# Performance work log

Hardware: AMD Instinct MI355X
Metric: run time of the kernel (lower is better)

## Reference

```python
import jax, jax.numpy as jnp
import numpy as np

N_TREES, N_LEAVES, PATH_LEN, N_NODES, D, B = 10, 16, 5, 31, 256, 4096


def _local_paths():
    # root-to-leaf paths of a full binary tree, depth 4: 31 nodes, 16 leaves, path len 5
    return np.array([[0, 1 + l // 8, 3 + l // 4, 7 + l // 2, 15 + l]
                     for l in range(N_LEAVES)], np.int32)


def setup_inputs() -> dict:
    key = jax.random.key(0)
    k1, k2, k3, k4, k5, k6 = jax.random.split(key, 6)
    # one activated leaf per tree -> multi-hot cross_features (B, N_TREES*N_LEAVES)
    leaf = jax.random.randint(k1, (B, N_TREES), 0, N_LEAVES)
    cross = jnp.zeros((B, N_TREES, N_LEAVES), jnp.float32)
    cross = cross.at[jnp.arange(B)[:, None], jnp.arange(N_TREES)[None, :], leaf].set(1.0)
    cross_features = cross.reshape(B, N_TREES * N_LEAVES)
    # learned params: node embedding table + single-layer LSTM (torch init scale 1/sqrt(D))
    emb = jax.random.normal(k2, (N_TREES * N_NODES, D), jnp.float32) * 0.02
    s = 1.0 / np.sqrt(D)
    W_ih = jax.random.uniform(k3, (4 * D, D), jnp.float32, -s, s)
    W_hh = jax.random.uniform(k4, (4 * D, D), jnp.float32, -s, s)
    b_ih = jax.random.uniform(k5, (4 * D,), jnp.float32, -s, s)
    b_hh = jax.random.uniform(k6, (4 * D,), jnp.float32, -s, s)
    return {"cross_features": cross_features, "emb": emb, "W_ih": W_ih,
            "W_hh": W_hh, "b_ih": b_ih, "b_hh": b_hh}


def reference(cross_features, emb, W_ih, W_hh, b_ih, b_hh):
    # global path node ids per (tree, leaf): [T, L, P]
    gpaths = jnp.asarray(_local_paths())[None, :, :] + \
        (jnp.arange(N_TREES, dtype=jnp.int32) * N_NODES)[:, None, None]
    # activated leaf per tree (exactly one hot per 16-leaf block)
    leaf = jnp.argmax(cross_features.reshape(B, N_TREES, N_LEAVES), axis=-1)  # [B, T]
    node_ids = gpaths[jnp.arange(N_TREES)[None, :], leaf]                     # [B, T, P]
    x = emb[node_ids].reshape(B * N_TREES, PATH_LEN, D)                       # packed paths
    # precompute input projections for all steps: [N, P, 4D]
    xg = jnp.einsum('npd,gd->npg', x, W_ih) + (b_ih + b_hh)

    def step(carry, xt):
        h, c = carry
        g = xt + h @ W_hh.T
        i, f, gg, o = jnp.split(g, 4, axis=-1)  # torch gate order: i, f, g, o
        c = jax.nn.sigmoid(f) * c + jax.nn.sigmoid(i) * jnp.tanh(gg)
        h = jax.nn.sigmoid(o) * jnp.tanh(c)
        return (h, c), None

    n = B * N_TREES
    h0 = jnp.zeros((n, D), x.dtype)
    (h, _), _ = jax.lax.scan(step, (h0, h0), jnp.swapaxes(xg, 0, 1))
    return h.reshape(B, N_TREES, D)
```

## Files before the change

### kernel.cpp

```cpp
#include <hip/hip_runtime.h>

#define NT 10
#define NL 16
#define NN 31
#define DD 256
#define G4 1024
#define NNODES (NT*NN)
#define NPATH (NT*NL)
#define NB 4096

__device__ unsigned g_tf[3][NT][32];

__device__ __forceinline__ float sigf(float x)   { return 1.0f / (1.0f + __expf(-x)); }
__device__ __forceinline__ float tanh_f(float x) { return 2.0f / (1.0f + __expf(-2.0f*x)) - 1.0f; }

__device__ __forceinline__ void co_store(float* p, float v) {
    union { float f; unsigned u; } c; c.f = v;
    __hip_atomic_store((unsigned*)p, c.u, __ATOMIC_RELAXED, __HIP_MEMORY_SCOPE_AGENT);
}

__global__ __launch_bounds__(256) void k_nodeproj(
    const float* __restrict__ emb, const float* __restrict__ Wih,
    const float* __restrict__ bih, const float* __restrict__ bhh,
    float* __restrict__ xg)
{
    __shared__ float smem[20 * 260 + 20 * 4 * 64];
    float4* es4 = (float4*)smem;
    float*  ps  = smem + 20 * 260;

    const int tid = threadIdx.x;
    const int nt  = blockIdx.x & 15;
    const int mt  = blockIdx.x >> 4;
    const int kq  = tid >> 6;
    const int w   = tid & 63;

    const float4* W4 = (const float4*)Wih + (size_t)(nt * 64 + w) * 64 + kq * 16;
    float4 wr[16];
    #pragma unroll
    for (int j = 0; j < 16; ++j) wr[j] = W4[j];

    const float4* emb4 = (const float4*)emb;
    #pragma unroll
    for (int r = 0; r < 5; ++r) {
        int idx = tid + 256 * r;
        int m = idx >> 6, q = idx & 63;
        int n = mt * 20 + m;
        es4[m * 65 + q] = (n < NNODES) ? emb4[(size_t)n * 64 + q]
                                       : make_float4(0.f, 0.f, 0.f, 0.f);
    }
    __syncthreads();

    float acc[20];
    #pragma unroll
    for (int m = 0; m < 20; ++m) acc[m] = 0.f;
    #pragma unroll
    for (int j = 0; j < 16; ++j) {
        float4 wv = wr[j];
        #pragma unroll
        for (int m = 0; m < 20; ++m) {
            float4 h = es4[m * 65 + kq * 16 + j];
            acc[m] = fmaf(wv.x, h.x, fmaf(wv.y, h.y,
                     fmaf(wv.z, h.z, fmaf(wv.w, h.w, acc[m]))));
        }
    }
    #pragma unroll
    for (int m = 0; m < 20; ++m) ps[(m * 4 + kq) * 64 + w] = acc[m];
    __syncthreads();

    const int nl   = tid & 63;
    const int msub = tid >> 6;
    const int j    = nt * 64 + nl;
    const float bsum = bih[j] + bhh[j];
    #pragma unroll
    for (int r = 0; r < 5; ++r) {
        int m = msub * 5 + r;
        int n = mt * 20 + m;
        float s = ps[(m * 4 + 0) * 64 + nl] + ps[(m * 4 + 1) * 64 + nl]
                + ps[(m * 4 + 2) * 64 + nl] + ps[(m * 4 + 3) * 64 + nl];
        if (n < NNODES) xg[(size_t)n * G4 + j] = s + bsum;
    }
}

__global__ __launch_bounds__(256) void k_treesteps(
    const float* __restrict__ xg, const float* __restrict__ Whh,
    float* __restrict__ h1g, float* __restrict__ h2g,
    float* __restrict__ h3g, float* __restrict__ h4g)
{
    __shared__ float hs[8 * DD];
    __shared__ float ps[8 * DD];
    __shared__ float cbuf[2][8 * 16];

    const int tid  = threadIdx.x;
    const int t    = blockIdx.x >> 4;
    const int dt   = blockIdx.x & 15;
    const int kq   = tid >> 6;
    const int w    = tid & 63;
    const int gate = w >> 4;
    const int col  = w & 15;

    const unsigned base = __hip_atomic_load(&g_tf[2][t][0],
        __ATOMIC_RELAXED, __HIP_MEMORY_SCOPE_AGENT);

    const float4* W4 = (const float4*)Whh
        + (size_t)(gate * DD + dt * 16 + col) * 64 + kq * 16;
    float4 wreg[16];
    #pragma unroll
    for (int j = 0; j < 16; ++j) wreg[j] = W4[j];

    float xnv[4][4];
    #pragma unroll
    for (int s = 1; s <= 4; ++s) {
        xnv[s-1][0] = 0.f; xnv[s-1][1] = 0.f;
        xnv[s-1][2] = 0.f; xnv[s-1][3] = 0.f;
        if (tid < (32 << (s - 1))) {
            int node = (1 << s) - 1 + (tid >> 4);
            const float* xn = xg + (size_t)(t * NN + node) * G4 + dt * 16 + (tid & 15);
            xnv[s-1][0] = xn[0];
            xnv[s-1][1] = xn[256];
            xnv[s-1][2] = xn[512];
            xnv[s-1][3] = xn[768];
        }
    }

    {
        const float* xr = xg + (size_t)(t * NN) * G4;
        float r_i = xr[tid], r_g = xr[512 + tid], r_o = xr[768 + tid];
        float c0 = sigf(r_i) * tanh_f(r_g);
        float h0 = sigf(r_o) * tanh_f(c0);
        hs[tid] = h0;
        if ((tid >> 4) == dt) cbuf[0][tid & 15] = c0;
    }
    __syncthreads();

    float* hout[3] = { h1g, h2g, h3g };
    const float* hin[3] = { h1g, h2g, h3g };

    #pragma unroll
    for (int s = 1; s <= 4; ++s) {
        const int L = 1 << (s - 1);

        if (s > 1) {
            if (tid < 64) {
                const unsigned tgt = base + 16u;
                while (__hip_atomic_load(&g_tf[s - 2][t][0],
                        __ATOMIC_RELAXED, __HIP_MEMORY_SCOPE_AGENT) < tgt)
                    __builtin_amdgcn_s_sleep(2);
            }
            __syncthreads();
            const unsigned long long* src =
                (const unsigned long long*)(hin[s - 2] + (size_t)t * L * DD);
            unsigned long long raw[4];
            #pragma unroll
            for (int r = 0; r < L / 2; ++r)
                raw[r] = __hip_atomic_load(src + tid + 256 * r,
                    __ATOMIC_RELAXED, __HIP_MEMORY_SCOPE_AGENT);
            float2* hs2 = (float2*)hs;
            #pragma unroll
            for (int r = 0; r < L / 2; ++r) {
                union { unsigned long long u; float2 f; } cv; cv.u = raw[r];
                hs2[tid + 256 * r] = cv.f;
            }
            __syncthreads();
        }

        const float4* hs4 = (const float4*)hs;
        float acc[8];
        #pragma unroll
        for (int p = 0; p < 8; ++p) acc[p] = 0.f;
        #pragma unroll
        for (int j = 0; j < 16; ++j) {
            float4 wv = wreg[j];
            #pragma unroll
            for (int p = 0; p < L; ++p) {
                float4 h = hs4[p * 64 + kq * 16 + j];
                acc[p] = fmaf(wv.x, h.x, fmaf(wv.y, h.y,
                         fmaf(wv.z, h.z, fmaf(wv.w, h.w, acc[p]))));
            }
        }
        #pragma unroll
        for (int p = 0; p < L; ++p) ps[p * DD + kq * 64 + w] = acc[p];
        __syncthreads();

        if (tid < 32 * L) {
            const int p  = tid >> 5;
            const int c2 = tid & 15;
            const int q  = tid >> 4;
            float g0 = 0.f, g1 = 0.f, g2 = 0.f, g3 = 0.f;
            #pragma unroll
            for (int k = 0; k < 4; ++k) {
                const float* pp = ps + p * DD + k * 64;
                g0 += pp[ 0 + c2]; g1 += pp[16 + c2];
                g2 += pp[32 + c2]; g3 += pp[48 + c2];
            }
            float gi = g0 + xnv[s - 1][0];
            float gf = g1 + xnv[s - 1][1];
            float gg = g2 + xnv[s - 1][2];
            float go = g3 + xnv[s - 1][3];
            float cin = cbuf[(s - 1) & 1][p * 16 + c2];
            float cn  = sigf(gf) * cin + sigf(gi) * tanh_f(gg);
            float hn  = sigf(go) * tanh_f(cn);
            if (s < 4) {
                cbuf[s & 1][q * 16 + c2] = cn;
                co_store(hout[s - 1] + (size_t)(t * 2 * L + q) * DD
                                     + dt * 16 + c2, hn);
            } else {
                h4g[(size_t)(t * NL + q) * DD + dt * 16 + c2] = hn;
            }
        }

        if (s < 4) {
            __syncthreads();
            if (tid == 0)
                __hip_atomic_fetch_add(&g_tf[s - 1][t][0], 1u,
                    __ATOMIC_RELAXED, __HIP_MEMORY_SCOPE_AGENT);
        }
    }
}

__global__ __launch_bounds__(256) void k_scatter(
    const float* __restrict__ cross, const float* __restrict__ htab,
    float* __restrict__ out)
{
    const int tid  = threadIdx.x;
    const int wave = tid >> 6;
    const int lane = tid & 63;
    const int r = blockIdx.x * 4 + wave;
    const int b = r / NT;
    const int t = r - b * NT;

    float v = 0.f;
    if (lane < NL) v = cross[(size_t)b * (NT * NL) + t * NL + lane];
    unsigned long long m = __ballot(v > 0.5f);
    int leaf = m ? (int)__builtin_ctzll(m) : 0;
    int p = t * NL + leaf;

    const float4* h4 = (const float4*)htab;
    float4* o4 = (float4*)out;
    o4[(size_t)r * 64 + lane] = h4[(size_t)p * 64 + lane];
}

extern "C" void kernel_launch(void* const* d_in, const int* in_sizes, int n_in,
                              void* d_out, int out_size, void* d_ws, size_t ws_size,
                              hipStream_t stream)
{
    const float* cross = (const float*)d_in[0];
    const float* emb   = (const float*)d_in[1];
    const float* Wih   = (const float*)d_in[2];
    const float* Whh   = (const float*)d_in[3];
    const float* bih   = (const float*)d_in[4];
    const float* bhh   = (const float*)d_in[5];
    float* out = (float*)d_out;

    float* ws = (float*)d_ws;
    float* xg = ws;
    float* h1 = xg + (size_t)NNODES * G4;
    float* h2 = h1 + 20 * DD;
    float* h3 = h2 + 40 * DD;
    float* h4 = h3 + 80 * DD;

    hipLaunchKernelGGL(k_nodeproj, dim3(256), dim3(256), 0, stream,
                       emb, Wih, bih, bhh, xg);
    hipLaunchKernelGGL(k_treesteps, dim3(160), dim3(256), 0, stream,
                       xg, Whh, h1, h2, h3, h4);
    hipLaunchKernelGGL(k_scatter, dim3(10240), dim3(256), 0, stream,
                       cross, h4, out);
}
```

Measured before the change: 111.8 us.

## Fuse node input projection into tree LSTM kernel with tagged-value flag sync

Merges the separate node-projection kernel into the tree-step kernel. Each block now computes the W_ih projection for its own tree's 31 nodes and gate slice into shared memory, which removes a launch and the global xg round trip. Cross-block synchronisation changes from per-level atomic counters to 64-bit stores that pack a generation tag with each hidden value, so consumers spin per element rather than on a counter. The cost is more registers per thread (both weight slices held) and more shared memory per block, plus per-element polling.

```diff
diff --git a/kernel.cpp b/kernel.cpp
--- a/kernel.cpp
+++ b/kernel.cpp
@@ -5,90 +5,37 @@
 #define NN 31
 #define DD 256
 #define G4 1024
-#define NNODES (NT*NN)
-#define NPATH (NT*NL)
 #define NB 4096
 
-__device__ unsigned g_tf[3][NT][32];
+__device__ unsigned g_gen[NT * 16];
 
 __device__ __forceinline__ float sigf(float x)   { return 1.0f / (1.0f + __expf(-x)); }
 __device__ __forceinline__ float tanh_f(float x) { return 2.0f / (1.0f + __expf(-2.0f*x)) - 1.0f; }
 
-__device__ __forceinline__ void co_store(float* p, float v) {
+__device__ __forceinline__ void pub64(unsigned long long* p, unsigned tag, float v) {
     union { float f; unsigned u; } c; c.f = v;
-    __hip_atomic_store((unsigned*)p, c.u, __ATOMIC_RELAXED, __HIP_MEMORY_SCOPE_AGENT);
-}
-
-__global__ __launch_bounds__(256) void k_nodeproj(
+    __hip_atomic_store(p, ((unsigned long long)tag << 32) | c.u,
+                       __ATOMIC_RELAXED, __HIP_MEMORY_SCOPE_AGENT);
+}
+__device__ __forceinline__ unsigned long long ld64(const unsigned long long* p) {
+    return __hip_atomic_load(p, __ATOMIC_RELAXED, __HIP_MEMORY_SCOPE_AGENT);
+}
+
+__global__ __launch_bounds__(256) void k_treelstm(
     const float* __restrict__ emb, const float* __restrict__ Wih,
-    const float* __restrict__ bih, const float* __restrict__ bhh,
-    float* __restrict__ xg)
+    const float* __restrict__ Whh, const float* __restrict__ bih,
+    const float* __restrict__ bhh,
+    unsigned long long* __restrict__ hx0, unsigned long long* __restrict__ hx1,
+    unsigned long long* __restrict__ hx2, unsigned long long* __restrict__ hx3,
+    float* __restrict__ h4g)
 {
-    __shared__ float smem[20 * 260 + 20 * 4 * 64];
-    float4* es4 = (float4*)smem;
-    float*  ps  = smem + 20 * 260;
-
-    const int tid = threadIdx.x;
-    const int nt  = blockIdx.x & 15;
-    const int mt  = blockIdx.x >> 4;
-    const int kq  = tid >> 6;
-    const int w   = tid & 63;
-
-    const float4* W4 = (const float4*)Wih + (size_t)(nt * 64 + w) * 64 + kq * 16;
-    float4 wr[16];
-    #pragma unroll
-    for (int j = 0; j < 16; ++j) wr[j] = W4[j];
-
-    const float4* emb4 = (const float4*)emb;
-    #pragma unroll
-    for (int r = 0; r < 5; ++r) {
-        int idx = tid + 256 * r;
-        int m = idx >> 6, q = idx & 63;
-        int n = mt * 20 + m;
-        es4[m * 65 + q] = (n < NNODES) ? emb4[(size_t)n * 64 + q]
-                                       : make_float4(0.f, 0.f, 0.f, 0.f);
-    }
-    __syncthreads();
-
-    float acc[20];
-    #pragma unroll
-    for (int m = 0; m < 20; ++m) acc[m] = 0.f;
-    #pragma unroll
-    for (int j = 0; j < 16; ++j) {
-        float4 wv = wr[j];
-        #pragma unroll
-        for (int m = 0; m < 20; ++m) {
-            float4 h = es4[m * 65 + kq * 16 + j];
-            acc[m] = fmaf(wv.x, h.x, fmaf(wv.y, h.y,
-                     fmaf(wv.z, h.z, fmaf(wv.w, h.w, acc[m]))));
-        }
-    }
-    #pragma unroll
-    for (int m = 0; m < 20; ++m) ps[(m * 4 + kq) * 64 + w] = acc[m];
-    __syncthreads();
-
-    const int nl   = tid & 63;
-    const int msub = tid >> 6;
-    const int j    = nt * 64 + nl;
-    const float bsum = bih[j] + bhh[j];
-    #pragma unroll
-    for (int r = 0; r < 5; ++r) {
-        int m = msub * 5 + r;
-        int n = mt * 20 + m;
-        float s = ps[(m * 4 + 0) * 64 + nl] + ps[(m * 4 + 1) * 64 + nl]
-                + ps[(m * 4 + 2) * 64 + nl] + ps[(m * 4 + 3) * 64 + nl];
-        if (n < NNODES) xg[(size_t)n * G4 + j] = s + bsum;
-    }
-}
-
-__global__ __launch_bounds__(256) void k_treesteps(
-    const float* __restrict__ xg, const float* __restrict__ Whh,
-    float* __restrict__ h1g, float* __restrict__ h2g,
-    float* __restrict__ h3g, float* __restrict__ h4g)
-{
-    __shared__ float hs[8 * DD];
-    __shared__ float ps[8 * DD];
-    __shared__ float cbuf[2][8 * 16];
+    __shared__ float es [NN * DD];
+    __shared__ float ps [8 * DD];
+    __shared__ float xsl[NN * 64];
+    __shared__ float hs [8 * DD];
+    __shared__ float cbuf[2 * 128];
+    __shared__ float bsl[64];
+    __shared__ unsigned stag;
 
     const int tid  = threadIdx.x;
     const int t    = blockIdx.x >> 4;
@@ -97,68 +44,114 @@
     const int w    = tid & 63;
     const int gate = w >> 4;
     const int col  = w & 15;
-
-    const unsigned base = __hip_atomic_load(&g_tf[2][t][0],
-        __ATOMIC_RELAXED, __HIP_MEMORY_SCOPE_AGENT);
-
-    const float4* W4 = (const float4*)Whh
-        + (size_t)(gate * DD + dt * 16 + col) * 64 + kq * 16;
-    float4 wreg[16];
-    #pragma unroll
-    for (int j = 0; j < 16; ++j) wreg[j] = W4[j];
-
-    float xnv[4][4];
-    #pragma unroll
-    for (int s = 1; s <= 4; ++s) {
-        xnv[s-1][0] = 0.f; xnv[s-1][1] = 0.f;
-        xnv[s-1][2] = 0.f; xnv[s-1][3] = 0.f;
-        if (tid < (32 << (s - 1))) {
-            int node = (1 << s) - 1 + (tid >> 4);
-            const float* xn = xg + (size_t)(t * NN + node) * G4 + dt * 16 + (tid & 15);
-            xnv[s-1][0] = xn[0];
-            xnv[s-1][1] = xn[256];
-            xnv[s-1][2] = xn[512];
-            xnv[s-1][3] = xn[768];
-        }
-    }
-
+    const int grow = gate * DD + dt * 16 + col;
+
+    if (tid == 0) {
+        unsigned G = __hip_atomic_load(&g_gen[t * 16 + dt],
+            __ATOMIC_RELAXED, __HIP_MEMORY_SCOPE_AGENT);
+        __hip_atomic_store(&g_gen[t * 16 + dt], G + 1u,
+            __ATOMIC_RELAXED, __HIP_MEMORY_SCOPE_AGENT);
+        stag = G + 1u;
+    }
+    if (tid < 64) {
+        int g2 = tid >> 4, c3 = tid & 15;
+        int r2 = g2 * DD + dt * 16 + c3;
+        bsl[tid] = bih[r2] + bhh[r2];
+    }
+
+    const float4* Wi4 = (const float4*)Wih + (size_t)grow * 64 + kq * 16;
+    const float4* Wh4 = (const float4*)Whh + (size_t)grow * 64 + kq * 16;
+    float4 wih[16], whh[16];
+    #pragma unroll
+    for (int j = 0; j < 16; ++j) { wih[j] = Wi4[j]; whh[j] = Wh4[j]; }
+
+    const float4* emb4 = (const float4*)emb + (size_t)t * NN * 64;
+    float4* es4 = (float4*)es;
+    #pragma unroll
+    for (int r = 0; r < 8; ++r) {
+        int idx = tid + 256 * r;
+        if (idx < NN * 64) es4[idx] = emb4[idx];
+    }
+    __syncthreads();
+    const unsigned tag = stag;
+
+    #pragma unroll
+    for (int b4 = 0; b4 < 4; ++b4) {
+        const int n0 = b4 * 8;
+        const int nn = (b4 == 3) ? 7 : 8;
+        float acc[8];
+        #pragma unroll
+        for (int m = 0; m < 8; ++m) acc[m] = 0.f;
+        #pragma unroll
+        for (int j = 0; j < 16; ++j) {
+            float4 wv = wih[j];
+            #pragma unroll
+            for (int m = 0; m < 8; ++m) {
+                if (m < nn) {
+                    float4 h = es4[(n0 + m) * 64 + kq * 16 + j];
+                    acc[m] = fmaf(wv.x, h.x, fmaf(wv.y, h.y,
+                             fmaf(wv.z, h.z, fmaf(wv.w, h.w, acc[m]))));
+                }
+            }
+        }
+        #pragma unroll
+        for (int m = 0; m < 8; ++m)
+            if (m < nn) ps[m * DD + kq * 64 + w] = acc[m];
+        __syncthreads();
+        #pragma unroll
+        for (int rep = 0; rep < 2; ++rep) {
+            int idx = tid + 256 * rep;
+            if (idx < nn * 64) {
+                int m = idx >> 6, w2 = idx & 63;
+                xsl[(n0 + m) * 64 + w2] =
+                      ps[m * DD +   0 + w2] + ps[m * DD +  64 + w2]
+                    + ps[m * DD + 128 + w2] + ps[m * DD + 192 + w2] + bsl[w2];
+            }
+        }
+        __syncthreads();
+    }
+
+    if (tid < 16) {
+        float xi  = xsl[ 0 + tid];
+        float xgg = xsl[32 + tid];
+        float xo  = xsl[48 + tid];
+        float c0 = sigf(xi) * tanh_f(xgg);
+        float h0 = sigf(xo) * tanh_f(c0);
+        cbuf[tid] = c0;
+        pub64(hx0 + (size_t)t * DD + dt * 16 + tid, tag, h0);
+    }
     {
-        const float* xr = xg + (size_t)(t * NN) * G4;
-        float r_i = xr[tid], r_g = xr[512 + tid], r_o = xr[768 + tid];
-        float c0 = sigf(r_i) * tanh_f(r_g);
-        float h0 = sigf(r_o) * tanh_f(c0);
-        hs[tid] = h0;
-        if ((tid >> 4) == dt) cbuf[0][tid & 15] = c0;
+        const unsigned long long* src = hx0 + (size_t)t * DD;
+        unsigned long long v = ld64(src + tid);
+        while ((unsigned)(v >> 32) != tag) {
+            __builtin_amdgcn_s_sleep(1);
+            v = ld64(src + tid);
+        }
+        union { unsigned u; float f; } cv; cv.u = (unsigned)v;
+        hs[tid] = cv.f;
     }
     __syncthreads();
 
-    float* hout[3] = { h1g, h2g, h3g };
-    const float* hin[3] = { h1g, h2g, h3g };
+    const unsigned long long* hin[3] = { hx1, hx2, hx3 };
+    unsigned long long* hout[3] = { hx1, hx2, hx3 };
 
     #pragma unroll
     for (int s = 1; s <= 4; ++s) {
         const int L = 1 << (s - 1);
 
         if (s > 1) {
-            if (tid < 64) {
-                const unsigned tgt = base + 16u;
-                while (__hip_atomic_load(&g_tf[s - 2][t][0],
-                        __ATOMIC_RELAXED, __HIP_MEMORY_SCOPE_AGENT) < tgt)
-                    __builtin_amdgcn_s_sleep(2);
-            }
-            __syncthreads();
-            const unsigned long long* src =
-                (const unsigned long long*)(hin[s - 2] + (size_t)t * L * DD);
-            unsigned long long raw[4];
-            #pragma unroll
-            for (int r = 0; r < L / 2; ++r)
-                raw[r] = __hip_atomic_load(src + tid + 256 * r,
-                    __ATOMIC_RELAXED, __HIP_MEMORY_SCOPE_AGENT);
-            float2* hs2 = (float2*)hs;
-            #pragma unroll
-            for (int r = 0; r < L / 2; ++r) {
-                union { unsigned long long u; float2 f; } cv; cv.u = raw[r];
-                hs2[tid + 256 * r] = cv.f;
+            const unsigned long long* src = hin[s - 2] + (size_t)t * L * DD;
+            unsigned long long v[8];
+            #pragma unroll
+            for (int r = 0; r < L; ++r) v[r] = ld64(src + tid + 256 * r);
+            #pragma unroll
+            for (int r = 0; r < L; ++r) {
+                while ((unsigned)(v[r] >> 32) != tag) {
+                    __builtin_amdgcn_s_sleep(1);
+                    v[r] = ld64(src + tid + 256 * r);
+                }
+                union { unsigned u; float f; } cv; cv.u = (unsigned)v[r];
+                hs[tid + 256 * r] = cv.f;
             }
             __syncthreads();
         }
@@ -169,7 +162,7 @@
         for (int p = 0; p < 8; ++p) acc[p] = 0.f;
         #pragma unroll
         for (int j = 0; j < 16; ++j) {
-            float4 wv = wreg[j];
+            float4 wv = whh[j];
             #pragma unroll
             for (int p = 0; p < L; ++p) {
                 float4 h = hs4[p * 64 + kq * 16 + j];
@@ -192,27 +185,22 @@
                 g0 += pp[ 0 + c2]; g1 += pp[16 + c2];
                 g2 += pp[32 + c2]; g3 += pp[48 + c2];
             }
-            float gi = g0 + xnv[s - 1][0];
-            float gf = g1 + xnv[s - 1][1];
-            float gg = g2 + xnv[s - 1][2];
-            float go = g3 + xnv[s - 1][3];
-            float cin = cbuf[(s - 1) & 1][p * 16 + c2];
+            const int node = (1 << s) - 1 + q;
+            const float* xp = xsl + node * 64;
+            float gi = g0 + xp[ 0 + c2];
+            float gf = g1 + xp[16 + c2];
+            float gg = g2 + xp[32 + c2];
+            float go = g3 + xp[48 + c2];
+            float cin = cbuf[((s - 1) & 1) * 128 + p * 16 + c2];
             float cn  = sigf(gf) * cin + sigf(gi) * tanh_f(gg);
             float hn  = sigf(go) * tanh_f(cn);
             if (s < 4) {
-                cbuf[s & 1][q * 16 + c2] = cn;
-                co_store(hout[s - 1] + (size_t)(t * 2 * L + q) * DD
-                                     + dt * 16 + c2, hn);
+                cbuf[(s & 1) * 128 + q * 16 + c2] = cn;
+                pub64(hout[s - 1] + (size_t)(t * 2 * L + q) * DD
+                                  + dt * 16 + c2, tag, hn);
             } else {
                 h4g[(size_t)(t * NL + q) * DD + dt * 16 + c2] = hn;
             }
-        }
-
-        if (s < 4) {
-            __syncthreads();
-            if (tid == 0)
-                __hip_atomic_fetch_add(&g_tf[s - 1][t][0], 1u,
-                    __ATOMIC_RELAXED, __HIP_MEMORY_SCOPE_AGENT);
         }
     }
 }
@@ -251,17 +239,14 @@
     const float* bhh   = (const float*)d_in[5];
     float* out = (float*)d_out;
 
-    float* ws = (float*)d_ws;
-    float* xg = ws;
-    float* h1 = xg + (size_t)NNODES * G4;
-    float* h2 = h1 + 20 * DD;
-    float* h3 = h2 + 40 * DD;
-    float* h4 = h3 + 80 * DD;
-
-    hipLaunchKernelGGL(k_nodeproj, dim3(256), dim3(256), 0, stream,
-                       emb, Wih, bih, bhh, xg);
-    hipLaunchKernelGGL(k_treesteps, dim3(160), dim3(256), 0, stream,
-                       xg, Whh, h1, h2, h3, h4);
+    unsigned long long* hx0 = (unsigned long long*)d_ws;
+    unsigned long long* hx1 = hx0 + (size_t)NT * DD;
+    unsigned long long* hx2 = hx1 + (size_t)2 * NT * DD;
+    unsigned long long* hx3 = hx2 + (size_t)4 * NT * DD;
+    float* h4g = (float*)(hx3 + (size_t)8 * NT * DD);
+
+    hipLaunchKernelGGL(k_treelstm, dim3(160), dim3(256), 0, stream,
+                       emb, Wih, Whh, bih, bhh, hx0, hx1, hx2, hx3, h4g);
     hipLaunchKernelGGL(k_scatter, dim3(10240), dim3(256), 0, stream,
-                       cross, h4, out);
-}
+                       cross, h4g, out);
+}
```

New measurement: 105.7 us. 1.06x faster.
